# Performance work log

Hardware: AMD Instinct MI355X
Metric: run time of the kernel (lower is better)

Reference implementation:

```python
import jax, jax.numpy as jnp
import numpy as np

B, N = 2, 1024
DIM = 1024
DQK = 128
NUM_KEYS = 256
NUM_MEM = NUM_KEYS * NUM_KEYS
TOPK = 32
RANK = 2
HEADS = 2
DV = 512
KCONV = 5
MARGIN = 0.15
AUX_W = 0.1
MEM_LR = 10.0
RMS_EPS = 1.1920929e-07  # torch.finfo(float32).eps (RMSNorm eps=None default)
LN_EPS = 1e-5


def setup_inputs() -> dict:
    key = jax.random.key(0)
    ks = jax.random.split(key, 6)
    return {
        "tokens": jax.random.normal(ks[0], (B, N, DIM), jnp.float32),
        "rms_w": jnp.ones((DIM,), jnp.float32),
        "conv_w": jax.random.normal(ks[1], (DIM, 1, KCONV), jnp.float32) * 0.1,
        "conv_b": jnp.zeros((DIM,), jnp.float32),
        "wq": jax.random.normal(ks[2], (DQK, DIM), jnp.float32) * 0.02,
        "qln_w": jnp.ones((DQK,), jnp.float32),
        "keys": jax.random.normal(ks[3], (2, RANK, NUM_KEYS, DQK), jnp.float32) * 0.01,
        "core": jax.random.normal(ks[4], (HEADS, RANK, RANK), jnp.float32) * 0.01,
        "memories": jax.random.normal(ks[5], (NUM_MEM, DV), jnp.float32) * 0.01,
    }


def _forward(tokens, rms_w, conv_w, conv_b, wq, qln_w, keys, core, memories):
    # prenorm RMSNorm
    x = tokens * jax.lax.rsqrt(jnp.mean(tokens * tokens, -1, keepdims=True) + RMS_EPS) * rms_w
    # SVD of core; rank-1 merge vectors (first left/right singular vectors)
    u, s, vh = jnp.linalg.svd(core, full_matrices=False)
    u_vec = u[..., :, 0]   # (H, R)
    t_vec = vh[..., 0, :]  # (H, R)  == v[..., :, 0]
    aux = jnp.sum(jnp.mean(jnp.square(jax.nn.relu(s[:, 1:] - MARGIN)), -1)) * AUX_W
    # causal depthwise conv (left-pad KCONV-1)
    xc = jnp.swapaxes(x, 1, 2)  # (B, D, N)
    xc = jax.lax.conv_general_dilated(
        xc, conv_w, (1,), [(KCONV - 1, 0)],
        feature_group_count=DIM, dimension_numbers=('NCH', 'OIH', 'NCH'))
    x = jnp.swapaxes(xc + conv_b[None, :, None], 1, 2)
    # queries + LayerNorm (no bias). NOTE: original applies key_ln but then uses
    # the raw self.keys in the einsum, so key normalization is a no-op; replicated.
    q = x @ wq.T
    mu = jnp.mean(q, -1, keepdims=True)
    var = jnp.mean(jnp.square(q - mu), -1, keepdims=True)
    q = (q - mu) * jax.lax.rsqrt(var + LN_EPS) * qln_w
    # product-key scores: (2, B, N, M, R)
    sc = jnp.einsum('bnd,crmd->cbnmr', q, keys)
    row_sc, col_sc = sc[0], sc[1]  # (B, N, M, R)
    m_row = jnp.einsum('bnmr,hr->hbnm', row_sc, u_vec)
    m_col = jnp.einsum('bnmr,hr->hbnm', col_sc, t_vec)
    _, top_row = jax.lax.top_k(m_row, TOPK)  # (H, B, N, K)
    _, top_col = jax.lax.top_k(m_col, TOPK)
    # candidate flat memory indices: outer sum -> (H, B, N, K*K)
    idx = (top_row * NUM_KEYS)[..., :, None] + top_col[..., None, :]
    idx = idx.reshape(HEADS, B, N, TOPK * TOPK)
    # gather per-rank scores at the top row/col keys
    rs = jnp.broadcast_to(row_sc[None], (HEADS,) + row_sc.shape)
    cs = jnp.broadcast_to(col_sc[None], (HEADS,) + col_sc.shape)
    ri = jnp.broadcast_to(top_row[..., None], top_row.shape + (RANK,))
    ci = jnp.broadcast_to(top_col[..., None], top_col.shape + (RANK,))
    f_row = jnp.take_along_axis(rs, ri, axis=3)  # (H, B, N, K, R)
    f_col = jnp.take_along_axis(cs, ci, axis=3)
    # bilinear core combine over ranks -> (H, B, N, K, K)
    scores = jnp.einsum('hbnir,hbnjs,hrs->hbnij', f_row, f_col, core)
    scores = scores.reshape(HEADS, B, N, TOPK * TOPK)
    fs, top_m = jax.lax.top_k(scores, TOPK)
    f_idx = jnp.take_along_axis(idx, top_m, axis=-1)  # (H, B, N, K)
    fs = jax.nn.sigmoid(fs)
    # gather from memory table: (H, B, N, K, DV)
    mem = memories[f_idx]
    # scale_gradient exactly as written: detach(t) - s*t + detach(s*t)  (grad = -s)
    scaled = mem * MEM_LR
    mem = jax.lax.stop_gradient(mem) - scaled + jax.lax.stop_gradient(scaled)
    agg = jnp.einsum('hbnkd,hbnk->hbnd', mem, fs)
    out = jnp.transpose(agg, (1, 2, 0, 3)).reshape(B, N, HEADS * DV)
    # combine_values_to_out is Identity (heads * dim_values == dim)
    return out, aux


def reference(tokens, rms_w, conv_w, conv_b, wq, qln_w, keys, core, memories):
    return _forward(tokens, rms_w, conv_w, conv_b, wq, qln_w, keys, core, memories)
```

## Files before the change

kernel.cpp:

```cpp
#include <hip/hip_runtime.h>
#include <math.h>


#define ROWS 2048
#define KSPLIT 8

__device__ inline double dsgn(double x, double y) { return (y >= 0.0) ? fabs(x) : -fabs(x); }

__device__ void dlasv2_dev(double f, double g, double h,
                           double& ssmin, double& ssmax,
                           double& snr, double& csr, double& snl, double& csl)
{
  const double EPSD = 2.2204460492503131e-16;
  double ft = f, fa = fabs(f), ht = h, ha = fabs(h);
  int pmax = 1;
  bool swp = (ha > fa);
  if (swp) { pmax = 3; double tp = ft; ft = ht; ht = tp; tp = fa; fa = ha; ha = tp; }
  double gt = g, ga = fabs(gt);
  double clt = 0.0, crt = 0.0, slt = 0.0, srt = 0.0;
  if (ga == 0.0) {
    ssmin = ha; ssmax = fa; clt = 1.0; crt = 1.0; slt = 0.0; srt = 0.0;
  } else {
    bool gasmal = true;
    if (ga > fa) {
      pmax = 2;
      if ((fa / ga) < EPSD) {
        gasmal = false;
        ssmax = ga;
        if (ha > 1.0) ssmin = fa / (ga / ha); else ssmin = (fa / ga) * ha;
        clt = 1.0; slt = ht / gt; srt = 1.0; crt = ft / gt;
      }
    }
    if (gasmal) {
      double dd = fa - ha, l;
      if (dd == fa) l = 1.0; else l = dd / fa;
      double m  = gt / ft;
      double t  = 2.0 - l;
      double mm = m * m, tt = t * t;
      double s  = sqrt(tt + mm);
      double r  = (l == 0.0) ? fabs(m) : sqrt(l * l + mm);
      double a  = 0.5 * (s + r);
      ssmin = ha / a;
      ssmax = fa * a;
      if (mm == 0.0) {
        if (l == 0.0) t = dsgn(2.0, ft) * dsgn(1.0, gt);
        else          t = gt / dsgn(dd, ft) + m / t;
      } else {
        t = (m / (s + t) + m / (r + l)) * (1.0 + a);
      }
      double ll = sqrt(t * t + 4.0);
      crt = 2.0 / ll;
      srt = t / ll;
      clt = (crt + srt * m) / a;
      slt = (ht / ft) * srt / a;
    }
  }
  if (swp) { csl = srt; snl = crt; csr = slt; snr = clt; }
  else     { csl = clt; snl = slt; csr = crt; snr = srt; }
  double tsign = 1.0;
  if (pmax == 1) tsign = dsgn(1.0, csr) * dsgn(1.0, csl) * dsgn(1.0, f);
  if (pmax == 2) tsign = dsgn(1.0, snr) * dsgn(1.0, csl) * dsgn(1.0, g);
  if (pmax == 3) tsign = dsgn(1.0, snr) * dsgn(1.0, snl) * dsgn(1.0, h);
  ssmax = dsgn(ssmax, tsign);
  ssmin = dsgn(ssmin, tsign * dsgn(1.0, f) * dsgn(1.0, h));
}

__device__ void do_svd(const float* __restrict__ core, float* __restrict__ misc,
                       float* __restrict__ aux_out)
{
  double aux = 0.0;
  for (int hh = 0; hh < 2; hh++) {
    double a = (double)core[hh * 4 + 0];
    double b = (double)core[hh * 4 + 1];
    double c = (double)core[hh * 4 + 2];
    double d = (double)core[hh * 4 + 3];
    double tau = 0.0, v2 = 0.0, d1, e, d2;
    if (c != 0.0) {
      double nrm  = sqrt(a * a + c * c);
      double beta = (a >= 0.0) ? -nrm : nrm;
      tau = (beta - a) / beta;
      v2  = c / (a - beta);
      double wsum = b + v2 * d;
      d1 = beta;
      e  = b - tau * wsum;
      d2 = d - tau * v2 * wsum;
    } else { d1 = a; e = b; d2 = d; }
    double ssmin, ssmax, snr, csr, snl, csl;
    dlasv2_dev(d1, e, d2, ssmin, ssmax, snr, csr, snl, csl);
    double t0 = csl + v2 * snl;
    double u0 = csl - tau * t0;
    double u1 = snl - tau * v2 * t0;
    double sg = (ssmax < 0.0) ? -1.0 : 1.0;
    misc[hh * 2 + 0]     = (float)u0;
    misc[hh * 2 + 1]     = (float)u1;
    misc[4 + hh * 2 + 0] = (float)(sg * csr);
    misc[4 + hh * 2 + 1] = (float)(sg * snr);
    double s2 = fabs(ssmin);
    double rl = s2 - 0.15; if (rl < 0.0) rl = 0.0;
    aux += rl * rl;
  }
  aux_out[0] = (float)(aux * 0.1);
}

__global__ __launch_bounds__(256) void rms_kernel(const float* __restrict__ tokens,
                                                  const float* __restrict__ core,
                                                  float* __restrict__ inv_sg,
                                                  float* __restrict__ misc,
                                                  float* __restrict__ aux_out)
{
  __shared__ float red[8][4];
  const int t    = threadIdx.x;
  const int row0 = blockIdx.x * 8;
  const int c0   = t * 4;
  float sq[8];
  #pragma unroll
  for (int s = 0; s < 8; s++) {
    float4 v = *(const float4*)(tokens + (size_t)(row0 + s) * 1024 + c0);
    sq[s] = v.x * v.x + v.y * v.y + v.z * v.z + v.w * v.w;
  }
  #pragma unroll
  for (int off = 32; off; off >>= 1) {
    #pragma unroll
    for (int s = 0; s < 8; s++) sq[s] += __shfl_down(sq[s], off, 64);
  }
  const int lane = t & 63, w = t >> 6;
  if (lane == 0) {
    #pragma unroll
    for (int s = 0; s < 8; s++) red[s][w] = sq[s];
  }
  __syncthreads();
  if (t < 8)
    inv_sg[row0 + t] = rsqrtf((red[t][0] + red[t][1] + red[t][2] + red[t][3])
                              * (1.0f / 1024.0f) + 1.1920929e-07f);
  if (blockIdx.x == 0 && t == 0) do_svd(core, misc, aux_out);
}

__global__ __launch_bounds__(256) void convgemm1_kernel(
    const float* __restrict__ tokens, const float* __restrict__ inv_sg,
    const float* __restrict__ rms_w,  const float* __restrict__ conv_w,
    const float* __restrict__ conv_b, const float* __restrict__ wq,
    float* __restrict__ qpart)
{
  __shared__ float xh[36 * 33];
  __shared__ __align__(16) float a_lds[32 * 32];
  __shared__ __align__(16) float b_lds[32 * 128];
  __shared__ float inv_l[36];
  const int t  = threadIdx.x;
  const int rb = blockIdx.x * 32;
  const int kb = blockIdx.y * 128;
  const int n0 = rb & 1023;

  if (t < 36) inv_l[t] = (n0 - 4 + t >= 0) ? inv_sg[rb - 4 + t] : 0.0f;

  const int tx = t & 31, ty = t >> 5;
  const int c0g = tx * 4, r0 = ty * 4;
  float acc[4][4];
  #pragma unroll
  for (int i = 0; i < 4; i++)
    #pragma unroll
    for (int j = 0; j < 4; j++) acc[i][j] = 0.0f;

  const int ob = t >> 1, kqb = (t & 1) * 16;
  const int cr = t & 31;
  const int ch = (t >> 5) * 4;

  for (int kt = 0; kt < 4; kt++) {
    const int k0 = kb + kt * 32;
    __syncthreads();
    #pragma unroll
    for (int it = 0; it < 2; it++) {
      int idx  = it * 256 + t;
      int srow = idx >> 3, f4 = (idx & 7) * 4;
      if (srow < 36) {
        float4 v = make_float4(0.f, 0.f, 0.f, 0.f);
        if (n0 - 4 + srow >= 0)
          v = *(const float4*)(tokens + (size_t)(rb - 4 + srow) * 1024 + k0 + f4);
        float iv = inv_l[srow];
        xh[srow * 33 + f4 + 0] = v.x * iv;
        xh[srow * 33 + f4 + 1] = v.y * iv;
        xh[srow * 33 + f4 + 2] = v.z * iv;
        xh[srow * 33 + f4 + 3] = v.w * iv;
      }
    }
    {
      const float* bp = wq + (size_t)ob * 1024 + k0 + kqb;
      float4 b0 = *(const float4*)(bp);
      float4 b1 = *(const float4*)(bp + 4);
      float4 b2 = *(const float4*)(bp + 8);
      float4 b3 = *(const float4*)(bp + 12);
      b_lds[(kqb +  0) * 128 + ob] = b0.x;  b_lds[(kqb +  1) * 128 + ob] = b0.y;
      b_lds[(kqb +  2) * 128 + ob] = b0.z;  b_lds[(kqb +  3) * 128 + ob] = b0.w;
      b_lds[(kqb +  4) * 128 + ob] = b1.x;  b_lds[(kqb +  5) * 128 + ob] = b1.y;
      b_lds[(kqb +  6) * 128 + ob] = b1.z;  b_lds[(kqb +  7) * 128 + ob] = b1.w;
      b_lds[(kqb +  8) * 128 + ob] = b2.x;  b_lds[(kqb +  9) * 128 + ob] = b2.y;
      b_lds[(kqb + 10) * 128 + ob] = b2.z;  b_lds[(kqb + 11) * 128 + ob] = b2.w;
      b_lds[(kqb + 12) * 128 + ob] = b3.x;  b_lds[(kqb + 13) * 128 + ob] = b3.y;
      b_lds[(kqb + 14) * 128 + ob] = b3.z;  b_lds[(kqb + 15) * 128 + ob] = b3.w;
    }
    __syncthreads();
    #pragma unroll
    for (int i = 0; i < 4; i++) {
      const int c = ch + i;
      const float* cw = conv_w + (size_t)(k0 + c) * 5;
      float a = xh[(cr + 0) * 33 + c] * cw[0]
              + xh[(cr + 1) * 33 + c] * cw[1]
              + xh[(cr + 2) * 33 + c] * cw[2]
              + xh[(cr + 3) * 33 + c] * cw[3]
              + xh[(cr + 4) * 33 + c] * cw[4];
      a_lds[c * 32 + cr] = a * rms_w[k0 + c] + conv_b[k0 + c];
    }
    __syncthreads();
    #pragma unroll
    for (int k = 0; k < 32; k++) {
      float4 av = *(const float4*)(a_lds + k * 32 + r0);
      float4 bv = *(const float4*)(b_lds + k * 128 + c0g);
      float ar[4] = {av.x, av.y, av.z, av.w};
      float br[4] = {bv.x, bv.y, bv.z, bv.w};
      #pragma unroll
      for (int i = 0; i < 4; i++)
        #pragma unroll
        for (int j = 0; j < 4; j++)
          acc[i][j] = fmaf(ar[i], br[j], acc[i][j]);
    }
  }
  float* C = qpart + (size_t)blockIdx.y * (ROWS * 128);
  #pragma unroll
  for (int i = 0; i < 4; i++) {
    float4 o4; o4.x = acc[i][0]; o4.y = acc[i][1]; o4.z = acc[i][2]; o4.w = acc[i][3];
    *(float4*)(C + (size_t)(rb + r0 + i) * 128 + c0g) = o4;
  }
}

__global__ __launch_bounds__(256) void gemm2ln_kernel(const float* __restrict__ qpart,
                                                      const float* __restrict__ qln_w,
                                                      const float* __restrict__ keys,
                                                      float* __restrict__ C)
{
  __shared__ __align__(16) float a_l[128 * 32];
  __shared__ __align__(16) float b_lds[32 * 128];
  const int t  = threadIdx.x;
  const int rb = blockIdx.x * 32;
  const int cb = blockIdx.y * 128;

  const int l32 = t & 31;
  const int g32 = t >> 5;
  float vs[4][4];
  #pragma unroll
  for (int j = 0; j < 4; j++) { vs[j][0]=0.f; vs[j][1]=0.f; vs[j][2]=0.f; vs[j][3]=0.f; }
  #pragma unroll
  for (int g = 0; g < KSPLIT; g++) {
    const float* pg = qpart + (size_t)g * (ROWS * 128) + (size_t)rb * 128 + l32 * 4;
    #pragma unroll
    for (int j = 0; j < 4; j++) {
      float4 v = *(const float4*)(pg + (g32 + 8 * j) * 128);
      vs[j][0] += v.x; vs[j][1] += v.y; vs[j][2] += v.z; vs[j][3] += v.w;
    }
  }
  float4 qw = *(const float4*)(qln_w + l32 * 4);
  #pragma unroll
  for (int j = 0; j < 4; j++) {
    float s1 = vs[j][0] + vs[j][1] + vs[j][2] + vs[j][3];
    #pragma unroll
    for (int off = 16; off; off >>= 1) s1 += __shfl_xor(s1, off, 32);
    float mu = s1 * (1.0f / 128.0f);
    float d0 = vs[j][0] - mu, d1 = vs[j][1] - mu, d2 = vs[j][2] - mu, d3 = vs[j][3] - mu;
    float s2 = d0 * d0 + d1 * d1 + d2 * d2 + d3 * d3;
    #pragma unroll
    for (int off = 16; off; off >>= 1) s2 += __shfl_xor(s2, off, 32);
    float rstd = rsqrtf(s2 * (1.0f / 128.0f) + 1e-5f);
    const int row = g32 + 8 * j;
    a_l[(l32 * 4 + 0) * 32 + row] = d0 * rstd * qw.x;
    a_l[(l32 * 4 + 1) * 32 + row] = d1 * rstd * qw.y;
    a_l[(l32 * 4 + 2) * 32 + row] = d2 * rstd * qw.z;
    a_l[(l32 * 4 + 3) * 32 + row] = d3 * rstd * qw.w;
  }
  __syncthreads();

  const int tx = t & 31, ty = t >> 5;
  const int c0 = tx * 4, r0 = ty * 4;
  float acc[4][4];
  #pragma unroll
  for (int i = 0; i < 4; i++)
    #pragma unroll
    for (int j = 0; j < 4; j++) acc[i][j] = 0.0f;

  const int ob = t >> 1, kqb = (t & 1) * 16;
  for (int kt = 0; kt < 4; kt++) {
    const int k0 = kt * 32;
    {
      const float* bp = keys + (size_t)(cb + ob) * 128 + k0 + kqb;
      float4 b0 = *(const float4*)(bp);
      float4 b1 = *(const float4*)(bp + 4);
      float4 b2 = *(const float4*)(bp + 8);
      float4 b3 = *(const float4*)(bp + 12);
      b_lds[(kqb +  0) * 128 + ob] = b0.x;  b_lds[(kqb +  1) * 128 + ob] = b0.y;
      b_lds[(kqb +  2) * 128 + ob] = b0.z;  b_lds[(kqb +  3) * 128 + ob] = b0.w;
      b_lds[(kqb +  4) * 128 + ob] = b1.x;  b_lds[(kqb +  5) * 128 + ob] = b1.y;
      b_lds[(kqb +  6) * 128 + ob] = b1.z;  b_lds[(kqb +  7) * 128 + ob] = b1.w;
      b_lds[(kqb +  8) * 128 + ob] = b2.x;  b_lds[(kqb +  9) * 128 + ob] = b2.y;
      b_lds[(kqb + 10) * 128 + ob] = b2.z;  b_lds[(kqb + 11) * 128 + ob] = b2.w;
      b_lds[(kqb + 12) * 128 + ob] = b3.x;  b_lds[(kqb + 13) * 128 + ob] = b3.y;
      b_lds[(kqb + 14) * 128 + ob] = b3.z;  b_lds[(kqb + 15) * 128 + ob] = b3.w;
    }
    __syncthreads();
    #pragma unroll
    for (int k = 0; k < 32; k++) {
      float4 av = *(const float4*)(a_l + (k0 + k) * 32 + r0);
      float4 bv = *(const float4*)(b_lds + k * 128 + c0);
      float ar[4] = {av.x, av.y, av.z, av.w};
      float br[4] = {bv.x, bv.y, bv.z, bv.w};
      #pragma unroll
      for (int i = 0; i < 4; i++)
        #pragma unroll
        for (int j = 0; j < 4; j++)
          acc[i][j] = fmaf(ar[i], br[j], acc[i][j]);
    }
    __syncthreads();
  }
  #pragma unroll
  for (int i = 0; i < 4; i++) {
    float4 o4; o4.x = acc[i][0]; o4.y = acc[i][1]; o4.z = acc[i][2]; o4.w = acc[i][3];
    *(float4*)(C + (size_t)(rb + r0 + i) * 1024 + cb + c0) = o4;
  }
}

__device__ inline unsigned f2ord(float f) {
  unsigned u = __float_as_uint(f);
  return (u & 0x80000000u) ? ~u : (u | 0x80000000u);
}
__device__ inline int lpc(unsigned long long m) {
  return __builtin_amdgcn_mbcnt_hi((unsigned)(m >> 32),
         __builtin_amdgcn_mbcnt_lo((unsigned)m, 0));
}

__global__ __launch_bounds__(256) void tail_kernel(const float* __restrict__ sc,
                                                   const float* __restrict__ misc,
                                                   const float* __restrict__ core,
                                                   const float* __restrict__ memories,
                                                   float* __restrict__ out)
{
  __shared__ __align__(16) float s_pl[1024];
  __shared__ int   tkbuf[4][32];
  __shared__ float mvals[4][32];
  __shared__ int   mcand[4][32];
  __shared__ int   s_idx[64];
  __shared__ float s_w[64];

  const int row = blockIdx.x;
  const int tid = threadIdx.x;
  ((float4*)s_pl)[tid] = ((const float4*)(sc + (size_t)row * 1024))[tid];
  __syncthreads();

  const int w = tid >> 6, lane = tid & 63;

  {
    const int h = w >> 1, side = w & 1;
    const float v0 = misc[side * 4 + h * 2 + 0];
    const float v1 = misc[side * 4 + h * 2 + 1];
    const float* p0 = s_pl + side * 512;
    const float* p1 = p0 + 256;
    const int mb = lane * 4;
    float4 a4 = *(const float4*)(p0 + mb);
    float4 b4 = *(const float4*)(p1 + mb);
    unsigned kk[4];
    kk[0] = f2ord(a4.x * v0 + b4.x * v1);
    kk[1] = f2ord(a4.y * v0 + b4.y * v1);
    kk[2] = f2ord(a4.z * v0 + b4.z * v1);
    kk[3] = f2ord(a4.w * v0 + b4.w * v1);
    unsigned tau = 0u;
    for (int b = 31; b >= 0; --b) {
      unsigned cand = tau | (1u << b);
      int cnt = 0;
      #pragma unroll
      for (int i = 0; i < 4; i++) cnt += __popcll(__ballot(kk[i] >= cand));
      if (cnt >= 32) {
        tau = cand;
        if (cnt == 32) break;
      }
    }
    unsigned long long bG[4], bE[4];
    int cntG = 0, sbG = 0, sbE = 0;
    #pragma unroll
    for (int i = 0; i < 4; i++) {
      bG[i] = __ballot(kk[i] > tau);
      bE[i] = __ballot(kk[i] == tau);
      cntG += __popcll(bG[i]);
      sbG  += lpc(bG[i]);
      sbE  += lpc(bE[i]);
    }
    const int need = 32 - cntG;
    int runG = 0, runE = 0;
    #pragma unroll
    for (int i = 0; i < 4; i++) {
      if (kk[i] > tau)       { tkbuf[w][sbG + runG] = mb + i; runG++; }
      else if (kk[i] == tau) {
        int r = sbE + runE;
        if (r < need) tkbuf[w][cntG + r] = mb + i;
        runE++;
      }
    }
  }
  __syncthreads();

  {
    const int h = w >> 1, half = w & 1;
    const float c00 = core[h * 4 + 0], c01 = core[h * 4 + 1];
    const float c10 = core[h * 4 + 2], c11 = core[h * 4 + 3];
    const int i_glob = half * 16 + (lane >> 2);
    const int ri = tkbuf[h * 2 + 0][i_glob];
    const float fr0 = s_pl[ri], fr1 = s_pl[256 + ri];
    const float a0 = fr0 * c00 + fr1 * c10;
    const float a1 = fr0 * c01 + fr1 * c11;
    const int j0 = (lane & 3) * 8;
    float sv[8];
    unsigned kk[8];
    #pragma unroll
    for (int t2 = 0; t2 < 8; t2++) {
      int cj = tkbuf[h * 2 + 1][j0 + t2];
      sv[t2] = a0 * s_pl[512 + cj] + a1 * s_pl[768 + cj];
      kk[t2] = f2ord(sv[t2]);
    }
    unsigned tau = 0u;
    for (int b = 31; b >= 0; --b) {
      unsigned cand = tau | (1u << b);
      int cnt = 0;
      #pragma unroll
      for (int i = 0; i < 8; i++) cnt += __popcll(__ballot(kk[i] >= cand));
      if (cnt >= 32) {
        tau = cand;
        if (cnt == 32) break;
      }
    }
    unsigned long long bG[8], bE[8];
    int cntG = 0, sbG = 0, sbE = 0;
    #pragma unroll
    for (int i = 0; i < 8; i++) {
      bG[i] = __ballot(kk[i] > tau);
      bE[i] = __ballot(kk[i] == tau);
      cntG += __popcll(bG[i]);
      sbG  += lpc(bG[i]);
      sbE  += lpc(bE[i]);
    }
    const int need = 32 - cntG;
    int runG = 0, runE = 0;
    #pragma unroll
    for (int i = 0; i < 8; i++) {
      int c = i_glob * 32 + j0 + i;
      if (kk[i] > tau) {
        mvals[w][sbG + runG] = sv[i]; mcand[w][sbG + runG] = c; runG++;
      } else if (kk[i] == tau) {
        int r = sbE + runE;
        if (r < need) { mvals[w][cntG + r] = sv[i]; mcand[w][cntG + r] = c; }
        runE++;
      }
    }
  }
  __syncthreads();

  if (w < 2) {
    const int h = w;
    const int half2 = lane >> 5, k = lane & 31;
    const float v = mvals[h * 2 + half2][k];
    const int   c = mcand[h * 2 + half2][k];
    int cnt = 0;
    #pragma unroll 8
    for (int j = 0; j < 64; j++) {
      float u = mvals[h * 2 + (j >> 5)][j & 31];
      int  uc = mcand[h * 2 + (j >> 5)][j & 31];
      cnt += (u > v || (u == v && uc < c)) ? 1 : 0;
    }
    if (cnt < 32) {
      int ii = c >> 5, jj = c & 31;
      s_idx[h * 32 + cnt] = tkbuf[h * 2][ii] * 256 + tkbuf[h * 2 + 1][jj];
      s_w[h * 32 + cnt]   = 1.0f / (1.0f + expf(-v));
    }
  }
  __syncthreads();

  const int h2 = tid >> 7;
  const int d4 = tid & 127;
  const int base = h2 * 32;
  const float* mb = memories + d4 * 4;
  float ax = 0.f, ay = 0.f, az = 0.f, aw = 0.f;
  float4 va[8], vb[8];
  float  wa[8], wb[8];
  #pragma unroll
  for (int i = 0; i < 8; i++) {
    int mi = s_idx[base + i]; wa[i] = s_w[base + i];
    va[i] = *(const float4*)(mb + (size_t)mi * 512);
  }
  #pragma unroll
  for (int i = 0; i < 8; i++) {
    int mi = s_idx[base + 8 + i]; wb[i] = s_w[base + 8 + i];
    vb[i] = *(const float4*)(mb + (size_t)mi * 512);
  }
  #pragma unroll
  for (int i = 0; i < 8; i++) {
    ax = fmaf(wa[i], va[i].x, ax); ay = fmaf(wa[i], va[i].y, ay);
    az = fmaf(wa[i], va[i].z, az); aw = fmaf(wa[i], va[i].w, aw);
  }
  #pragma unroll
  for (int i = 0; i < 8; i++) {
    int mi = s_idx[base + 16 + i]; wa[i] = s_w[base + 16 + i];
    va[i] = *(const float4*)(mb + (size_t)mi * 512);
  }
  #pragma unroll
  for (int i = 0; i < 8; i++) {
    ax = fmaf(wb[i], vb[i].x, ax); ay = fmaf(wb[i], vb[i].y, ay);
    az = fmaf(wb[i], vb[i].z, az); aw = fmaf(wb[i], vb[i].w, aw);
  }
  #pragma unroll
  for (int i = 0; i < 8; i++) {
    int mi = s_idx[base + 24 + i]; wb[i] = s_w[base + 24 + i];
    vb[i] = *(const float4*)(mb + (size_t)mi * 512);
  }
  #pragma unroll
  for (int i = 0; i < 8; i++) {
    ax = fmaf(wa[i], va[i].x, ax); ay = fmaf(wa[i], va[i].y, ay);
    az = fmaf(wa[i], va[i].z, az); aw = fmaf(wa[i], va[i].w, aw);
  }
  #pragma unroll
  for (int i = 0; i < 8; i++) {
    ax = fmaf(wb[i], vb[i].x, ax); ay = fmaf(wb[i], vb[i].y, ay);
    az = fmaf(wb[i], vb[i].z, az); aw = fmaf(wb[i], vb[i].w, aw);
  }
  float4 o4; o4.x = ax; o4.y = ay; o4.z = az; o4.w = aw;
  ((float4*)out)[(size_t)row * 256 + tid] = o4;
}

extern "C" void kernel_launch(void* const* d_in, const int* in_sizes, int n_in,
                              void* d_out, int out_size, void* d_ws, size_t ws_size,
                              hipStream_t stream) {
  const float* tokens = (const float*)d_in[0];
  const float* rms_w  = (const float*)d_in[1];
  const float* conv_w = (const float*)d_in[2];
  const float* conv_b = (const float*)d_in[3];
  const float* wq     = (const float*)d_in[4];
  const float* qln_w  = (const float*)d_in[5];
  const float* keys   = (const float*)d_in[6];
  const float* core   = (const float*)d_in[7];
  const float* mems   = (const float*)d_in[8];
  float* out = (float*)d_out;
  float* ws  = (float*)d_ws;

  float* misc  = ws;
  float* invs  = ws + 1024;
  float* qpart = ws + 4096;
  float* sc    = qpart + 2097152;

  rms_kernel     <<<ROWS / 8, 256, 0, stream>>>(tokens, core, invs, misc,
                                                out + 2097152);
  convgemm1_kernel<<<dim3(64, KSPLIT), 256, 0, stream>>>(tokens, invs, rms_w,
                                                         conv_w, conv_b, wq, qpart);
  gemm2ln_kernel <<<dim3(64, 8), 256, 0, stream>>>(qpart, qln_w, keys, sc);
  tail_kernel    <<<ROWS, 256, 0, stream>>>(sc, misc, core, mems, out);
}
```

Before: 272.9 us.

## Process four rows per tail block, overlapping memory gathers with next-row selection

```diff
diff --git a/kernel.cpp b/kernel.cpp
--- a/kernel.cpp
+++ b/kernel.cpp
@@ -333,26 +333,12 @@
          __builtin_amdgcn_mbcnt_lo((unsigned)m, 0));
 }
 
-__global__ __launch_bounds__(256) void tail_kernel(const float* __restrict__ sc,
-                                                   const float* __restrict__ misc,
-                                                   const float* __restrict__ core,
-                                                   const float* __restrict__ memories,
-                                                   float* __restrict__ out)
-{
-  __shared__ __align__(16) float s_pl[1024];
-  __shared__ int   tkbuf[4][32];
-  __shared__ float mvals[4][32];
-  __shared__ int   mcand[4][32];
-  __shared__ int   s_idx[64];
-  __shared__ float s_w[64];
-
-  const int row = blockIdx.x;
-  const int tid = threadIdx.x;
-  ((float4*)s_pl)[tid] = ((const float4*)(sc + (size_t)row * 1024))[tid];
-  __syncthreads();
-
-  const int w = tid >> 6, lane = tid & 63;
-
+__device__ __forceinline__ void select_token(
+    const float* s_pl, const float* __restrict__ misc,
+    const float* __restrict__ core,
+    int (*tkbuf)[32], float (*mvals)[32], int (*mcand)[32],
+    int* s_idx, float* s_w, int w, int lane)
+{
   {
     const int h = w >> 1, side = w & 1;
     const float v0 = misc[side * 4 + h * 2 + 0];
@@ -476,56 +462,59 @@
     }
   }
   __syncthreads();
+}
+
+__global__ __launch_bounds__(256) void tail_kernel(const float* __restrict__ sc,
+                                                   const float* __restrict__ misc,
+                                                   const float* __restrict__ core,
+                                                   const float* __restrict__ memories,
+                                                   float* __restrict__ out)
+{
+  __shared__ __align__(16) float s_pl4[4][1024];
+  __shared__ int   tkbuf[4][32];
+  __shared__ float mvals[4][32];
+  __shared__ int   mcand[4][32];
+  __shared__ int   s_idx[2][64];
+  __shared__ float s_w[2][64];
+
+  const int row0 = blockIdx.x * 4;
+  const int tid  = threadIdx.x;
+  const int w = tid >> 6, lane = tid & 63;
+
+  #pragma unroll
+  for (int r = 0; r < 4; r++)
+    ((float4*)s_pl4[r])[tid] = ((const float4*)(sc + (size_t)(row0 + r) * 1024))[tid];
+  __syncthreads();
+
+  select_token(s_pl4[0], misc, core, tkbuf, mvals, mcand, s_idx[0], s_w[0], w, lane);
 
   const int h2 = tid >> 7;
   const int d4 = tid & 127;
-  const int base = h2 * 32;
-  const float* mb = memories + d4 * 4;
-  float ax = 0.f, ay = 0.f, az = 0.f, aw = 0.f;
-  float4 va[8], vb[8];
-  float  wa[8], wb[8];
-  #pragma unroll
-  for (int i = 0; i < 8; i++) {
-    int mi = s_idx[base + i]; wa[i] = s_w[base + i];
-    va[i] = *(const float4*)(mb + (size_t)mi * 512);
-  }
-  #pragma unroll
-  for (int i = 0; i < 8; i++) {
-    int mi = s_idx[base + 8 + i]; wb[i] = s_w[base + 8 + i];
-    vb[i] = *(const float4*)(mb + (size_t)mi * 512);
-  }
-  #pragma unroll
-  for (int i = 0; i < 8; i++) {
-    ax = fmaf(wa[i], va[i].x, ax); ay = fmaf(wa[i], va[i].y, ay);
-    az = fmaf(wa[i], va[i].z, az); aw = fmaf(wa[i], va[i].w, aw);
-  }
-  #pragma unroll
-  for (int i = 0; i < 8; i++) {
-    int mi = s_idx[base + 16 + i]; wa[i] = s_w[base + 16 + i];
-    va[i] = *(const float4*)(mb + (size_t)mi * 512);
-  }
-  #pragma unroll
-  for (int i = 0; i < 8; i++) {
-    ax = fmaf(wb[i], vb[i].x, ax); ay = fmaf(wb[i], vb[i].y, ay);
-    az = fmaf(wb[i], vb[i].z, az); aw = fmaf(wb[i], vb[i].w, aw);
-  }
-  #pragma unroll
-  for (int i = 0; i < 8; i++) {
-    int mi = s_idx[base + 24 + i]; wb[i] = s_w[base + 24 + i];
-    vb[i] = *(const float4*)(mb + (size_t)mi * 512);
-  }
-  #pragma unroll
-  for (int i = 0; i < 8; i++) {
-    ax = fmaf(wa[i], va[i].x, ax); ay = fmaf(wa[i], va[i].y, ay);
-    az = fmaf(wa[i], va[i].z, az); aw = fmaf(wa[i], va[i].w, aw);
-  }
-  #pragma unroll
-  for (int i = 0; i < 8; i++) {
-    ax = fmaf(wb[i], vb[i].x, ax); ay = fmaf(wb[i], vb[i].y, ay);
-    az = fmaf(wb[i], vb[i].z, az); aw = fmaf(wb[i], vb[i].w, aw);
-  }
-  float4 o4; o4.x = ax; o4.y = ay; o4.z = az; o4.w = aw;
-  ((float4*)out)[(size_t)row * 256 + tid] = o4;
+  const int gbase = h2 * 32;
+  const float* mp = memories + d4 * 4;
+
+  #pragma unroll
+  for (int rr = 0; rr < 4; rr++) {
+    const int buf = rr & 1;
+    float4 va[32];
+    #pragma unroll
+    for (int i = 0; i < 32; i++) {
+      int mi = s_idx[buf][gbase + i];
+      va[i] = *(const float4*)(mp + (size_t)mi * 512);
+    }
+    if (rr < 3)
+      select_token(s_pl4[rr + 1], misc, core, tkbuf, mvals, mcand,
+                   s_idx[buf ^ 1], s_w[buf ^ 1], w, lane);
+    float ax = 0.f, ay = 0.f, az = 0.f, aw = 0.f;
+    #pragma unroll
+    for (int i = 0; i < 32; i++) {
+      float wt = s_w[buf][gbase + i];
+      ax = fmaf(wt, va[i].x, ax); ay = fmaf(wt, va[i].y, ay);
+      az = fmaf(wt, va[i].z, az); aw = fmaf(wt, va[i].w, aw);
+    }
+    float4 o4; o4.x = ax; o4.y = ay; o4.z = az; o4.w = aw;
+    ((float4*)out)[(size_t)(row0 + rr) * 256 + tid] = o4;
+  }
 }
 
 extern "C" void kernel_launch(void* const* d_in, const int* in_sizes, int n_in,
@@ -553,5 +542,5 @@
   convgemm1_kernel<<<dim3(64, KSPLIT), 256, 0, stream>>>(tokens, invs, rms_w,
                                                          conv_w, conv_b, wq, qpart);
   gemm2ln_kernel <<<dim3(64, 8), 256, 0, stream>>>(qpart, qln_w, keys, sc);
-  tail_kernel    <<<ROWS, 256, 0, stream>>>(sc, misc, core, mems, out);
-}
+  tail_kernel    <<<ROWS / 4, 256, 0, stream>>>(sc, misc, core, mems, out);
+}
```

After: 280.8 us. +2.9%, slower.

## Split tail kernel blocks per head to double grid parallelism

Applied to the files above, without the earlier changes.

```diff
diff --git a/kernel.cpp b/kernel.cpp
--- a/kernel.cpp
+++ b/kernel.cpp
@@ -340,21 +340,22 @@
                                                    float* __restrict__ out)
 {
   __shared__ __align__(16) float s_pl[1024];
-  __shared__ int   tkbuf[4][32];
-  __shared__ float mvals[4][32];
-  __shared__ int   mcand[4][32];
-  __shared__ int   s_idx[64];
-  __shared__ float s_w[64];
-
-  const int row = blockIdx.x;
+  __shared__ int   tkbuf[2][32];
+  __shared__ float mvals[2][32];
+  __shared__ int   mcand[2][32];
+  __shared__ int   s_idx[32];
+  __shared__ float s_w[32];
+
+  const int bid = blockIdx.x;
+  const int row = bid >> 1, h = bid & 1;
   const int tid = threadIdx.x;
   ((float4*)s_pl)[tid] = ((const float4*)(sc + (size_t)row * 1024))[tid];
   __syncthreads();
 
   const int w = tid >> 6, lane = tid & 63;
 
-  {
-    const int h = w >> 1, side = w & 1;
+  if (w < 2) {
+    const int side = w;
     const float v0 = misc[side * 4 + h * 2 + 0];
     const float v1 = misc[side * 4 + h * 2 + 1];
     const float* p0 = s_pl + side * 512;
@@ -392,22 +393,22 @@
     int runG = 0, runE = 0;
     #pragma unroll
     for (int i = 0; i < 4; i++) {
-      if (kk[i] > tau)       { tkbuf[w][sbG + runG] = mb + i; runG++; }
+      if (kk[i] > tau)       { tkbuf[side][sbG + runG] = mb + i; runG++; }
       else if (kk[i] == tau) {
         int r = sbE + runE;
-        if (r < need) tkbuf[w][cntG + r] = mb + i;
+        if (r < need) tkbuf[side][cntG + r] = mb + i;
         runE++;
       }
     }
   }
   __syncthreads();
 
-  {
-    const int h = w >> 1, half = w & 1;
+  if (w < 2) {
+    const int half = w;
     const float c00 = core[h * 4 + 0], c01 = core[h * 4 + 1];
     const float c10 = core[h * 4 + 2], c11 = core[h * 4 + 3];
     const int i_glob = half * 16 + (lane >> 2);
-    const int ri = tkbuf[h * 2 + 0][i_glob];
+    const int ri = tkbuf[0][i_glob];
     const float fr0 = s_pl[ri], fr1 = s_pl[256 + ri];
     const float a0 = fr0 * c00 + fr1 * c10;
     const float a1 = fr0 * c01 + fr1 * c11;
@@ -416,7 +417,7 @@
     unsigned kk[8];
     #pragma unroll
     for (int t2 = 0; t2 < 8; t2++) {
-      int cj = tkbuf[h * 2 + 1][j0 + t2];
+      int cj = tkbuf[1][j0 + t2];
       sv[t2] = a0 * s_pl[512 + cj] + a1 * s_pl[768 + cj];
       kk[t2] = f2ord(sv[t2]);
     }
@@ -447,85 +448,77 @@
     for (int i = 0; i < 8; i++) {
       int c = i_glob * 32 + j0 + i;
       if (kk[i] > tau) {
-        mvals[w][sbG + runG] = sv[i]; mcand[w][sbG + runG] = c; runG++;
+        mvals[half][sbG + runG] = sv[i]; mcand[half][sbG + runG] = c; runG++;
       } else if (kk[i] == tau) {
         int r = sbE + runE;
-        if (r < need) { mvals[w][cntG + r] = sv[i]; mcand[w][cntG + r] = c; }
+        if (r < need) { mvals[half][cntG + r] = sv[i]; mcand[half][cntG + r] = c; }
         runE++;
       }
     }
   }
   __syncthreads();
 
-  if (w < 2) {
-    const int h = w;
+  if (w == 0) {
     const int half2 = lane >> 5, k = lane & 31;
-    const float v = mvals[h * 2 + half2][k];
-    const int   c = mcand[h * 2 + half2][k];
+    const float v = mvals[half2][k];
+    const int   c = mcand[half2][k];
     int cnt = 0;
     #pragma unroll 8
     for (int j = 0; j < 64; j++) {
-      float u = mvals[h * 2 + (j >> 5)][j & 31];
-      int  uc = mcand[h * 2 + (j >> 5)][j & 31];
+      float u = mvals[j >> 5][j & 31];
+      int  uc = mcand[j >> 5][j & 31];
       cnt += (u > v || (u == v && uc < c)) ? 1 : 0;
     }
     if (cnt < 32) {
       int ii = c >> 5, jj = c & 31;
-      s_idx[h * 32 + cnt] = tkbuf[h * 2][ii] * 256 + tkbuf[h * 2 + 1][jj];
-      s_w[h * 32 + cnt]   = 1.0f / (1.0f + expf(-v));
+      s_idx[cnt] = tkbuf[0][ii] * 256 + tkbuf[1][jj];
+      s_w[cnt]   = 1.0f / (1.0f + expf(-v));
     }
   }
   __syncthreads();
 
-  const int h2 = tid >> 7;
-  const int d4 = tid & 127;
-  const int base = h2 * 32;
-  const float* mb = memories + d4 * 4;
-  float ax = 0.f, ay = 0.f, az = 0.f, aw = 0.f;
-  float4 va[8], vb[8];
+  const float* mp = memories + tid * 2;
+  float ax = 0.f, ay = 0.f;
+  float2 va[8], vb[8];
   float  wa[8], wb[8];
   #pragma unroll
   for (int i = 0; i < 8; i++) {
-    int mi = s_idx[base + i]; wa[i] = s_w[base + i];
-    va[i] = *(const float4*)(mb + (size_t)mi * 512);
-  }
-  #pragma unroll
-  for (int i = 0; i < 8; i++) {
-    int mi = s_idx[base + 8 + i]; wb[i] = s_w[base + 8 + i];
-    vb[i] = *(const float4*)(mb + (size_t)mi * 512);
+    int mi = s_idx[i]; wa[i] = s_w[i];
+    va[i] = *(const float2*)(mp + (size_t)mi * 512);
+  }
+  #pragma unroll
+  for (int i = 0; i < 8; i++) {
+    int mi = s_idx[8 + i]; wb[i] = s_w[8 + i];
+    vb[i] = *(const float2*)(mp + (size_t)mi * 512);
   }
   #pragma unroll
   for (int i = 0; i < 8; i++) {
     ax = fmaf(wa[i], va[i].x, ax); ay = fmaf(wa[i], va[i].y, ay);
-    az = fmaf(wa[i], va[i].z, az); aw = fmaf(wa[i], va[i].w, aw);
-  }
-  #pragma unroll
-  for (int i = 0; i < 8; i++) {
-    int mi = s_idx[base + 16 + i]; wa[i] = s_w[base + 16 + i];
-    va[i] = *(const float4*)(mb + (size_t)mi * 512);
+  }
+  #pragma unroll
+  for (int i = 0; i < 8; i++) {
+    int mi = s_idx[16 + i]; wa[i] = s_w[16 + i];
+    va[i] = *(const float2*)(mp + (size_t)mi * 512);
   }
   #pragma unroll
   for (int i = 0; i < 8; i++) {
     ax = fmaf(wb[i], vb[i].x, ax); ay = fmaf(wb[i], vb[i].y, ay);
-    az = fmaf(wb[i], vb[i].z, az); aw = fmaf(wb[i], vb[i].w, aw);
-  }
-  #pragma unroll
-  for (int i = 0; i < 8; i++) {
-    int mi = s_idx[base + 24 + i]; wb[i] = s_w[base + 24 + i];
-    vb[i] = *(const float4*)(mb + (size_t)mi * 512);
+  }
+  #pragma unroll
+  for (int i = 0; i < 8; i++) {
+    int mi = s_idx[24 + i]; wb[i] = s_w[24 + i];
+    vb[i] = *(const float2*)(mp + (size_t)mi * 512);
   }
   #pragma unroll
   for (int i = 0; i < 8; i++) {
     ax = fmaf(wa[i], va[i].x, ax); ay = fmaf(wa[i], va[i].y, ay);
-    az = fmaf(wa[i], va[i].z, az); aw = fmaf(wa[i], va[i].w, aw);
   }
   #pragma unroll
   for (int i = 0; i < 8; i++) {
     ax = fmaf(wb[i], vb[i].x, ax); ay = fmaf(wb[i], vb[i].y, ay);
-    az = fmaf(wb[i], vb[i].z, az); aw = fmaf(wb[i], vb[i].w, aw);
-  }
-  float4 o4; o4.x = ax; o4.y = ay; o4.z = az; o4.w = aw;
-  ((float4*)out)[(size_t)row * 256 + tid] = o4;
+  }
+  float2 o2; o2.x = ax; o2.y = ay;
+  *(float2*)(out + (size_t)row * 1024 + h * 512 + tid * 2) = o2;
 }
 
 extern "C" void kernel_launch(void* const* d_in, const int* in_sizes, int n_in,
@@ -553,5 +546,5 @@
   convgemm1_kernel<<<dim3(64, KSPLIT), 256, 0, stream>>>(tokens, invs, rms_w,
                                                          conv_w, conv_b, wq, qpart);
   gemm2ln_kernel <<<dim3(64, 8), 256, 0, stream>>>(qpart, qln_w, keys, sc);
-  tail_kernel    <<<ROWS, 256, 0, stream>>>(sc, misc, core, mems, out);
-}
+  tail_kernel    <<<ROWS * 2, 256, 0, stream>>>(sc, misc, core, mems, out);
+}
```

After: 295.4 us. 1.08x slower.
